# Optimization experiments

Measured on AMD Instinct MI355X. Metric: run time of the kernel, lower is better.

## Reference

```python
import jax, jax.numpy as jnp
import numpy as np

STRIDE = 2
PADDING = 1


def setup_inputs() -> dict:
    key = jax.random.key(0)
    k1, k2, k3, k4, k5 = jax.random.split(key, 5)
    B, C, H, W = 32, 128, 64, 64
    O, kh, kw = 256, 3, 3
    ah = H + 2 * PADDING - (kh - 1)  # 64
    oh = ah // STRIDE                # 32 (divisible -> ceil == floor, rest == 0)
    inputs = {
        "input": jax.random.normal(k1, (B, C, H, W), dtype=jnp.float32),
        "weight": jax.random.normal(k2, (O, C, kh, kw), dtype=jnp.float32) * 0.05,
        "bias": jax.random.normal(k3, (O,), dtype=jnp.float32) * 0.05,
        "selh": jax.random.randint(k4, (oh, oh), 0, STRIDE, dtype=jnp.int32),
        "selw": jax.random.randint(k5, (oh, oh), 0, STRIDE, dtype=jnp.int32),
    }
    return inputs


def reference(input, weight, bias, selh, selw):
    # Faithful to SConv2dAvg.forward with stoch=True, mask == -1, stride=2:
    # unfold(input, k, pad, stride=1) -> stochastic gather of one position per
    # stride x stride cell (offsets selh/selw) -> GEMM with flattened weight -> reshape.
    B, C, H, W = input.shape
    O, _, kh, kw = weight.shape
    ah = H + 2 * PADDING - (kh - 1)
    aw = W + 2 * PADDING - (kw - 1)
    oh = ah // STRIDE  # divisible by construction; ceil_mode correction is a no-op
    ow = aw // STRIDE
    xp = jnp.pad(input, ((0, 0), (0, 0), (PADDING, PADDING), (PADDING, PADDING)))
    # selected unfold positions in the afterconv grid
    rng_h = selh + (jnp.arange(oh, dtype=selh.dtype) * STRIDE)[:, None]   # [oh, ow]
    rng_w = selw + (jnp.arange(ow, dtype=selw.dtype) * STRIDE)[None, :]   # [oh, ow]
    # gather k x k patches directly (equivalent to gathering unfold columns)
    rows = rng_h[:, :, None, None] + jnp.arange(kh)[None, None, :, None]  # [oh, ow, kh, 1]
    cols = rng_w[:, :, None, None] + jnp.arange(kw)[None, None, None, :]  # [oh, ow, 1, kw]
    patches = xp[:, :, rows, cols]  # [B, C, oh, ow, kh, kw]
    out = jnp.einsum('bchwij,ocij->bohw', patches, weight) + bias[None, :, None, None]
    return out  # [B, O, oh, ow]
```

## Files before the change

kernel.cpp:

```cpp
#include <hip/hip_runtime.h>
#include <hip/hip_bf16.h>


typedef short bf16x8 __attribute__((ext_vector_type(8)));
typedef float f32x4  __attribute__((ext_vector_type(4)));

#define NSTEP 36
#define WPRE_BYTES (NSTEP * 256 * 32 * 2)
#define TRANS_BYTES (32 * 66 * 66 * 128 * 2)
#define TOTAL_WS (WPRE_BYTES + TRANS_BYTES)

__device__ __forceinline__ unsigned short f2bf(float x) {
  unsigned u = __float_as_uint(x);
  return (unsigned short)((u + 0x7fffu + ((u >> 16) & 1u)) >> 16);
}
__device__ __forceinline__ unsigned pk2(float a, float b) {
  unsigned ua = __float_as_uint(a), ub = __float_as_uint(b);
  return ((ua + 0x7fffu + ((ua >> 16) & 1u)) >> 16) |
         ((ub + 0x7fffu + ((ub >> 16) & 1u)) & 0xffff0000u);
}
__device__ __forceinline__ bf16x8 ld_frag(const uint4* a) {
  union { uint4 u; bf16x8 s; } cv; cv.u = *a; return cv.s;
}
__device__ __forceinline__ void async16(const void* g, void* l) {
  __builtin_amdgcn_global_load_lds(
      (__attribute__((address_space(1))) void*)(void*)g,
      (__attribute__((address_space(3))) void*)l, 16, 0, 0);
}

__global__ __launch_bounds__(256) void prep(const float* __restrict__ in,
                                            const float* __restrict__ w,
                                            unsigned short* __restrict__ tp,
                                            unsigned short* __restrict__ wpre) {
  const int tid = threadIdx.x;
  if (blockIdx.x >= 66) {
    const int s    = blockIdx.x - 66;
    const int o    = (blockIdx.y << 3) + (tid >> 5);
    const int k_in = tid & 31;
    const int kg   = (s << 5) + (((k_in >> 3) ^ ((o >> 1) & 3)) << 3) + (k_in & 7);
    const int tap  = kg >> 7;
    const int c    = kg & 127;
    const int di   = (tap >= 6) ? 2 : ((tap >= 3) ? 1 : 0);
    const int dj   = tap - di * 3;
    wpre[(s << 13) + (o << 5) + k_in] = f2bf(w[(o * 128 + c) * 9 + di * 3 + dj]);
    return;
  }
  __shared__ float lds[128 * 65];
  const int hp = blockIdx.x;
  const int b  = blockIdx.y;
  uint4* rowp = (uint4*)(tp + (size_t)(b * 66 + hp) * 66 * 128);
  uint4 z; z.x = z.y = z.z = z.w = 0u;
  if (hp == 0 || hp == 65) {
    for (int s = tid; s < 1056; s += 256) rowp[s] = z;
    return;
  }
  const int h = hp - 1;
  const float* src = in + ((size_t)b << 19) + (h << 6);
  const int ww4 = (tid & 15) << 2;
  const int c0  = tid >> 4;
#pragma unroll
  for (int pass = 0; pass < 8; ++pass) {
    int c = (pass << 4) + c0;
    float4 v = *(const float4*)(src + ((size_t)c << 12) + ww4);
    float* lp = lds + c * 65 + ww4;
    lp[0] = v.x; lp[1] = v.y; lp[2] = v.z; lp[3] = v.w;
  }
  __syncthreads();
  for (int s = tid; s < 1056; s += 256) {
    if (s < 16 || s >= 1040) { rowp[s] = z; continue; }
    int idx = s - 16;
    int wq = idx >> 4, c8 = idx & 15;
    const float* lp = lds + (c8 << 3) * 65 + wq;
    uint4 d;
    d.x = pk2(lp[0],   lp[65]);
    d.y = pk2(lp[130], lp[195]);
    d.z = pk2(lp[260], lp[325]);
    d.w = pk2(lp[390], lp[455]);
    rowp[s] = d;
  }
}

__global__ __launch_bounds__(512, 4) void sconv_mfma4(
    const unsigned short* __restrict__ tp,
    const unsigned short* __restrict__ wpre,
    const float* __restrict__ bias,
    const int* __restrict__ selh,
    const int* __restrict__ selw,
    float* __restrict__ out)
{
  __shared__ uint4 Alds[4][512];
  __shared__ uint4 Blds[4][512];
  __shared__ float bias_s[128];

  const int tid = threadIdx.x;
  const int d0    = blockIdx.x;
  const int blk   = ((d0 & 7) << 6) + (d0 >> 3);
  const int b     = blk >> 4;
  const int y0    = ((blk >> 1) & 7) << 2;
  const int ohalf = blk & 1;

  if (tid < 128) bias_s[tid] = bias[(ohalf << 7) + tid];

  const int p0 = tid >> 2;
  const int sl = tid & 3;
  int addr0;
  {
    const int py = y0 + (p0 >> 5);
    const int px = p0 & 31;
    addr0 = (b * 66 + 2 * py + selh[(py << 5) | px]) * 66
          + 2 * px + selw[(py << 5) | px];
  }
  const int u0 = sl ^ ((p0 >> 1) & 3);
  const char* tbase = (const char*)tp;

  const int wv = tid >> 6, ln = tid & 63;
  const int wo = wv & 1;
  const int wp = wv >> 1;
  const int lo = ln & 15, hi = ln >> 4;

  const char* wsrc = (const char*)wpre + (ohalf << 13) + (tid << 4);

  f32x4 acc[4][2] = {};

#define STAGE(BUF, KK)                                                        \
  do {                                                                        \
    const int tap_ = (KK) >> 2;                                               \
    const int di_  = (tap_ >= 6) ? 2 : ((tap_ >= 3) ? 1 : 0);                 \
    const int dj_  = tap_ - 3 * di_;                                          \
    const int toff_ = ((di_ * 66 + dj_) << 8) + (((KK) & 3) << 6) + (u0 << 4);\
    async16(tbase + ((size_t)addr0 << 8) + toff_, &Alds[BUF][wv << 6]);       \
    async16(wsrc + ((KK) << 14), &Blds[BUF][wv << 6]);                        \
  } while (0)

#define DO_MMA(BUF)                                                           \
  do {                                                                        \
    const uint4* A_ = &Alds[BUF][0];                                          \
    const uint4* B_ = &Blds[BUF][0];                                          \
    bf16x8 FW[4], FP[2];                                                      \
    _Pragma("unroll")                                                         \
    for (int f = 0; f < 4; ++f) {                                             \
      const int orow = (wo << 6) + (f << 4) + lo;                             \
      FW[f] = ld_frag(B_ + (orow << 2) + (hi ^ ((orow >> 1) & 3)));           \
    }                                                                         \
    _Pragma("unroll")                                                         \
    for (int f = 0; f < 2; ++f) {                                             \
      const int prow = (wp << 5) + (f << 4) + lo;                             \
      FP[f] = ld_frag(A_ + (prow << 2) + (hi ^ ((prow >> 1) & 3)));           \
    }                                                                         \
    _Pragma("unroll")                                                         \
    for (int fo = 0; fo < 4; ++fo)                                            \
      _Pragma("unroll")                                                       \
      for (int fp = 0; fp < 2; ++fp)                                          \
        acc[fo][fp] = __builtin_amdgcn_mfma_f32_16x16x32_bf16(                \
            FW[fo], FP[fp], acc[fo][fp], 0, 0, 0);                            \
  } while (0)

  STAGE(0, 0);
  STAGE(1, 1);

#pragma unroll 4
  for (int kk = 0; kk < NSTEP - 2; ++kk) {
    STAGE((kk + 2) & 3, kk + 2);
    asm volatile("s_waitcnt vmcnt(4)" ::: "memory");
    __builtin_amdgcn_s_barrier();
    asm volatile("" ::: "memory");
    DO_MMA(kk & 3);
    asm volatile("s_waitcnt lgkmcnt(0)" ::: "memory");
  }

  asm volatile("s_waitcnt vmcnt(2)" ::: "memory");
  __builtin_amdgcn_s_barrier();
  asm volatile("" ::: "memory");
  DO_MMA(2);
  asm volatile("s_waitcnt lgkmcnt(0)" ::: "memory");

  asm volatile("s_waitcnt vmcnt(0)" ::: "memory");
  __builtin_amdgcn_s_barrier();
  asm volatile("" ::: "memory");
  DO_MMA(3);
#undef STAGE
#undef DO_MMA

  float* ob = out + ((size_t)b << 18) + ((size_t)ohalf << 17) + (y0 << 5);
#pragma unroll
  for (int fo = 0; fo < 4; ++fo) {
    const int obase = (wo << 6) + (fo << 4) + (hi << 2);
#pragma unroll
    for (int fp = 0; fp < 2; ++fp) {
      const int pix = (wp << 5) + (fp << 4) + lo;
#pragma unroll
      for (int j = 0; j < 4; ++j) {
        const int o = obase + j;
        ob[((size_t)o << 10) + pix] = acc[fo][fp][j] + bias_s[o];
      }
    }
  }
}

__global__ __launch_bounds__(256) void sconv_naive(
    const float* __restrict__ in, const float* __restrict__ w,
    const float* __restrict__ bias, const int* __restrict__ selh,
    const int* __restrict__ selw, float* __restrict__ out) {
  int idx = (blockIdx.x << 8) + threadIdx.x;
  if (idx >= 32 * 256 * 32 * 32) return;
  int x = idx & 31, y = (idx >> 5) & 31, o = (idx >> 10) & 255, b = idx >> 18;
  int rh0 = 2 * y + selh[(y << 5) | x] - 1;
  int rw0 = 2 * x + selw[(y << 5) | x] - 1;
  const float* inb = in + ((size_t)b << 19);
  const float* wo_ = w + o * 1152;
  float acc = bias[o];
  for (int c = 0; c < 128; ++c)
    for (int i = 0; i < 3; ++i) {
      int rh = rh0 + i;
      if (rh < 0 || rh >= 64) continue;
      for (int j = 0; j < 3; ++j) {
        int rw = rw0 + j;
        if (rw < 0 || rw >= 64) continue;
        acc += inb[(c << 12) + (rh << 6) + rw] * wo_[c * 9 + i * 3 + j];
      }
    }
  out[idx] = acc;
}

extern "C" void kernel_launch(void* const* d_in, const int* in_sizes, int n_in,
                              void* d_out, int out_size, void* d_ws, size_t ws_size,
                              hipStream_t stream) {
  const float* in   = (const float*)d_in[0];
  const float* w    = (const float*)d_in[1];
  const float* bias = (const float*)d_in[2];
  const int*   selh = (const int*)d_in[3];
  const int*   selw = (const int*)d_in[4];
  float* out = (float*)d_out;

  if (ws_size >= (size_t)TOTAL_WS) {
    unsigned short* wpre = (unsigned short*)d_ws;
    unsigned short* tp   = (unsigned short*)((char*)d_ws + WPRE_BYTES);
    prep<<<dim3(102, 32), dim3(256), 0, stream>>>(in, w, tp, wpre);
    sconv_mfma4<<<dim3(512), dim3(512), 0, stream>>>(tp, wpre, bias, selh, selw, out);
  } else {
    sconv_naive<<<dim3(32768), dim3(256), 0, stream>>>(in, w, bias, selh, selw, out);
  }
}
```

Baseline: 45.31 us.

## Halve block threads and double per-wave MFMA tile with priority boost

Shrinks each block from 8 to 4 waves, with every wave now covering a 64x64 output tile (4x4 MFMA fragments) instead of 64x32. Each thread issues two A and two B async loads per stage, and the wait counts are doubled to match. The change raises operand reuse per LDS fragment load and adds s_setprio around the MFMA burst to favour math issue. In exchange it uses more accumulator registers per wave and leaves fewer waves per block to hide latency.

```diff
diff --git a/kernel.cpp b/kernel.cpp
--- a/kernel.cpp
+++ b/kernel.cpp
@@ -80,7 +80,7 @@
   }
 }
 
-__global__ __launch_bounds__(512, 4) void sconv_mfma4(
+__global__ __launch_bounds__(256, 2) void sconv_mfma5(
     const unsigned short* __restrict__ tp,
     const unsigned short* __restrict__ wpre,
     const float* __restrict__ bias,
@@ -101,58 +101,66 @@
 
   if (tid < 128) bias_s[tid] = bias[(ohalf << 7) + tid];
 
-  const int p0 = tid >> 2;
-  const int sl = tid & 3;
-  int addr0;
+  const int wv = tid >> 6, ln = tid & 63;
+
+  size_t asrc0, asrc1;
   {
-    const int py = y0 + (p0 >> 5);
-    const int px = p0 & 31;
-    addr0 = (b * 66 + 2 * py + selh[(py << 5) | px]) * 66
-          + 2 * px + selw[(py << 5) | px];
-  }
-  const int u0 = sl ^ ((p0 >> 1) & 3);
+    const int c4 = ln & 3;
+#pragma unroll
+    for (int r = 0; r < 2; ++r) {
+      const int p  = (wv << 5) + (r << 4) + (ln >> 2);
+      const int py = y0 + (p >> 5);
+      const int px = p & 31;
+      const int addr = (b * 66 + 2 * py + selh[(py << 5) | px]) * 66
+                     + 2 * px + selw[(py << 5) | px];
+      const int u = c4 ^ ((p >> 1) & 3);
+      const size_t v = ((size_t)addr << 8) + (u << 4);
+      if (r == 0) asrc0 = v; else asrc1 = v;
+    }
+  }
   const char* tbase = (const char*)tp;
-
-  const int wv = tid >> 6, ln = tid & 63;
-  const int wo = wv & 1;
-  const int wp = wv >> 1;
+  const char* wB = (const char*)wpre + (ohalf << 13) + ((wv << 1) << 10) + (ln << 4);
+
+  const int wo = wv & 1, wp = wv >> 1;
   const int lo = ln & 15, hi = ln >> 4;
 
-  const char* wsrc = (const char*)wpre + (ohalf << 13) + (tid << 4);
-
-  f32x4 acc[4][2] = {};
+  f32x4 acc[4][4] = {};
 
 #define STAGE(BUF, KK)                                                        \
   do {                                                                        \
     const int tap_ = (KK) >> 2;                                               \
     const int di_  = (tap_ >= 6) ? 2 : ((tap_ >= 3) ? 1 : 0);                 \
     const int dj_  = tap_ - 3 * di_;                                          \
-    const int toff_ = ((di_ * 66 + dj_) << 8) + (((KK) & 3) << 6) + (u0 << 4);\
-    async16(tbase + ((size_t)addr0 << 8) + toff_, &Alds[BUF][wv << 6]);       \
-    async16(wsrc + ((KK) << 14), &Blds[BUF][wv << 6]);                        \
+    const int toff_ = ((di_ * 66 + dj_) << 8) + (((KK) & 3) << 6);            \
+    async16(tbase + asrc0 + toff_, &Alds[BUF][(wv << 1) << 6]);               \
+    async16(tbase + asrc1 + toff_, &Alds[BUF][((wv << 1) + 1) << 6]);         \
+    async16(wB + ((KK) << 14),        &Blds[BUF][(wv << 1) << 6]);            \
+    async16(wB + ((KK) << 14) + 1024, &Blds[BUF][((wv << 1) + 1) << 6]);      \
   } while (0)
 
 #define DO_MMA(BUF)                                                           \
   do {                                                                        \
     const uint4* A_ = &Alds[BUF][0];                                          \
     const uint4* B_ = &Blds[BUF][0];                                          \
-    bf16x8 FW[4], FP[2];                                                      \
+    bf16x8 FW[4], FP[4];                                                      \
     _Pragma("unroll")                                                         \
     for (int f = 0; f < 4; ++f) {                                             \
       const int orow = (wo << 6) + (f << 4) + lo;                             \
       FW[f] = ld_frag(B_ + (orow << 2) + (hi ^ ((orow >> 1) & 3)));           \
     }                                                                         \
     _Pragma("unroll")                                                         \
-    for (int f = 0; f < 2; ++f) {                                             \
-      const int prow = (wp << 5) + (f << 4) + lo;                             \
+    for (int f = 0; f < 4; ++f) {                                             \
+      const int prow = (wp << 6) + (f << 4) + lo;                             \
       FP[f] = ld_frag(A_ + (prow << 2) + (hi ^ ((prow >> 1) & 3)));           \
     }                                                                         \
+    __builtin_amdgcn_s_setprio(1);                                            \
     _Pragma("unroll")                                                         \
     for (int fo = 0; fo < 4; ++fo)                                            \
       _Pragma("unroll")                                                       \
-      for (int fp = 0; fp < 2; ++fp)                                          \
+      for (int fp = 0; fp < 4; ++fp)                                          \
         acc[fo][fp] = __builtin_amdgcn_mfma_f32_16x16x32_bf16(                \
             FW[fo], FP[fp], acc[fo][fp], 0, 0, 0);                            \
+    __builtin_amdgcn_s_setprio(0);                                            \
   } while (0)
 
   STAGE(0, 0);
@@ -161,14 +169,14 @@
 #pragma unroll 4
   for (int kk = 0; kk < NSTEP - 2; ++kk) {
     STAGE((kk + 2) & 3, kk + 2);
-    asm volatile("s_waitcnt vmcnt(4)" ::: "memory");
+    asm volatile("s_waitcnt vmcnt(8)" ::: "memory");
     __builtin_amdgcn_s_barrier();
     asm volatile("" ::: "memory");
     DO_MMA(kk & 3);
     asm volatile("s_waitcnt lgkmcnt(0)" ::: "memory");
   }
 
-  asm volatile("s_waitcnt vmcnt(2)" ::: "memory");
+  asm volatile("s_waitcnt vmcnt(4)" ::: "memory");
   __builtin_amdgcn_s_barrier();
   asm volatile("" ::: "memory");
   DO_MMA(2);
@@ -186,8 +194,8 @@
   for (int fo = 0; fo < 4; ++fo) {
     const int obase = (wo << 6) + (fo << 4) + (hi << 2);
 #pragma unroll
-    for (int fp = 0; fp < 2; ++fp) {
-      const int pix = (wp << 5) + (fp << 4) + lo;
+    for (int fp = 0; fp < 4; ++fp) {
+      const int pix = (wp << 6) + (fp << 4) + lo;
 #pragma unroll
       for (int j = 0; j < 4; ++j) {
         const int o = obase + j;
@@ -236,7 +244,7 @@
     unsigned short* wpre = (unsigned short*)d_ws;
     unsigned short* tp   = (unsigned short*)((char*)d_ws + WPRE_BYTES);
     prep<<<dim3(102, 32), dim3(256), 0, stream>>>(in, w, tp, wpre);
-    sconv_mfma4<<<dim3(512), dim3(512), 0, stream>>>(tp, wpre, bias, selh, selw, out);
+    sconv_mfma5<<<dim3(512), dim3(256), 0, stream>>>(tp, wpre, bias, selh, selw, out);
   } else {
     sconv_naive<<<dim3(32768), dim3(256), 0, stream>>>(in, w, bias, selh, selw, out);
   }
```

After: 46.11 us. No clear change (+1.8%).

## Load activation fragments directly into registers, dropping the LDS A-tile

Applied to the files above, without the earlier changes.

The gathered activation operand is no longer staged through shared memory. Each lane loads its two MFMA input fragments straight from global memory into registers, double-buffered across k-steps, while weights still go through the async LDS ring. This removes the LDS writes and reads for A and cuts shared memory use. It also raises MFMA priority via s_setprio. The cost is more global loads that are less coalesced, with the 8 waves re-fetching overlapping data, and waitcnt accounting that must now cover both streams.

```diff
diff --git a/kernel.cpp b/kernel.cpp
--- a/kernel.cpp
+++ b/kernel.cpp
@@ -80,7 +80,7 @@
   }
 }
 
-__global__ __launch_bounds__(512, 4) void sconv_mfma4(
+__global__ __launch_bounds__(512, 4) void sconv_mfma6(
     const unsigned short* __restrict__ tp,
     const unsigned short* __restrict__ wpre,
     const float* __restrict__ bias,
@@ -88,7 +88,6 @@
     const int* __restrict__ selw,
     float* __restrict__ out)
 {
-  __shared__ uint4 Alds[4][512];
   __shared__ uint4 Blds[4][512];
   __shared__ float bias_s[128];
 
@@ -101,84 +100,103 @@
 
   if (tid < 128) bias_s[tid] = bias[(ohalf << 7) + tid];
 
-  const int p0 = tid >> 2;
-  const int sl = tid & 3;
-  int addr0;
-  {
-    const int py = y0 + (p0 >> 5);
-    const int px = p0 & 31;
-    addr0 = (b * 66 + 2 * py + selh[(py << 5) | px]) * 66
-          + 2 * px + selw[(py << 5) | px];
-  }
-  const int u0 = sl ^ ((p0 >> 1) & 3);
-  const char* tbase = (const char*)tp;
-
   const int wv = tid >> 6, ln = tid & 63;
   const int wo = wv & 1;
   const int wp = wv >> 1;
   const int lo = ln & 15, hi = ln >> 4;
 
-  const char* wsrc = (const char*)wpre + (ohalf << 13) + (tid << 4);
+  size_t apix0, apix1;
+  {
+#pragma unroll
+    for (int f = 0; f < 2; ++f) {
+      const int P  = (wp << 5) + (f << 4) + lo;
+      const int py = y0 + (P >> 5);
+      const int px = P & 31;
+      const int addr = (b * 66 + 2 * py + selh[(py << 5) | px]) * 66
+                     + 2 * px + selw[(py << 5) | px];
+      const size_t v = ((size_t)addr << 8) + (hi << 4);
+      if (f == 0) apix0 = v; else apix1 = v;
+    }
+  }
+  const char* tbase = (const char*)tp;
+  const char* wB = (const char*)wpre + (ohalf << 13) + (tid << 4);
 
   f32x4 acc[4][2] = {};
 
-#define STAGE(BUF, KK)                                                        \
+#define TOFF(KK) (((((KK) >> 2) >= 6 ? 2 : (((KK) >> 2) >= 3 ? 1 : 0)) * 66    \
+                   + (((KK) >> 2) - 3 * (((KK) >> 2) >= 6 ? 2                  \
+                                          : (((KK) >> 2) >= 3 ? 1 : 0)))) << 8)\
+                  + (((KK) & 3) << 6)
+
+#define LOADA(S0, S1, KK)                                                     \
   do {                                                                        \
-    const int tap_ = (KK) >> 2;                                               \
-    const int di_  = (tap_ >= 6) ? 2 : ((tap_ >= 3) ? 1 : 0);                 \
-    const int dj_  = tap_ - 3 * di_;                                          \
-    const int toff_ = ((di_ * 66 + dj_) << 8) + (((KK) & 3) << 6) + (u0 << 4);\
-    async16(tbase + ((size_t)addr0 << 8) + toff_, &Alds[BUF][wv << 6]);       \
-    async16(wsrc + ((KK) << 14), &Blds[BUF][wv << 6]);                        \
+    const int to_ = TOFF(KK);                                                 \
+    S0 = *(const bf16x8*)(tbase + apix0 + to_);                               \
+    S1 = *(const bf16x8*)(tbase + apix1 + to_);                               \
   } while (0)
 
-#define DO_MMA(BUF)                                                           \
+#define STAGE_B(KK) async16(wB + ((KK) << 14), &Blds[(KK) & 3][tid >> 2 << 2]  \
+                            + (tid & 3))
+
+#define DO_MMA(BUF, S0, S1)                                                   \
   do {                                                                        \
-    const uint4* A_ = &Alds[BUF][0];                                          \
     const uint4* B_ = &Blds[BUF][0];                                          \
-    bf16x8 FW[4], FP[2];                                                      \
+    bf16x8 FW[4];                                                             \
     _Pragma("unroll")                                                         \
     for (int f = 0; f < 4; ++f) {                                             \
       const int orow = (wo << 6) + (f << 4) + lo;                             \
       FW[f] = ld_frag(B_ + (orow << 2) + (hi ^ ((orow >> 1) & 3)));           \
     }                                                                         \
+    __builtin_amdgcn_s_setprio(1);                                            \
     _Pragma("unroll")                                                         \
-    for (int f = 0; f < 2; ++f) {                                             \
-      const int prow = (wp << 5) + (f << 4) + lo;                             \
-      FP[f] = ld_frag(A_ + (prow << 2) + (hi ^ ((prow >> 1) & 3)));           \
+    for (int fo = 0; fo < 4; ++fo) {                                          \
+      acc[fo][0] = __builtin_amdgcn_mfma_f32_16x16x32_bf16(                   \
+          FW[fo], S0, acc[fo][0], 0, 0, 0);                                   \
+      acc[fo][1] = __builtin_amdgcn_mfma_f32_16x16x32_bf16(                   \
+          FW[fo], S1, acc[fo][1], 0, 0, 0);                                   \
     }                                                                         \
-    _Pragma("unroll")                                                         \
-    for (int fo = 0; fo < 4; ++fo)                                            \
-      _Pragma("unroll")                                                       \
-      for (int fp = 0; fp < 2; ++fp)                                          \
-        acc[fo][fp] = __builtin_amdgcn_mfma_f32_16x16x32_bf16(                \
-            FW[fo], FP[fp], acc[fo][fp], 0, 0, 0);                            \
+    __builtin_amdgcn_s_setprio(0);                                            \
   } while (0)
 
-  STAGE(0, 0);
-  STAGE(1, 1);
-
-#pragma unroll 4
-  for (int kk = 0; kk < NSTEP - 2; ++kk) {
-    STAGE((kk + 2) & 3, kk + 2);
-    asm volatile("s_waitcnt vmcnt(4)" ::: "memory");
+  bf16x8 FPa0, FPa1, FPb0, FPb1;
+
+  STAGE_B(0);
+  LOADA(FPa0, FPa1, 0);
+  STAGE_B(1);
+
+#pragma unroll 2
+  for (int kk = 0; kk < NSTEP - 2; kk += 2) {
+    LOADA(FPb0, FPb1, kk + 1);
+    STAGE_B(kk + 2);
+    asm volatile("s_waitcnt vmcnt(6)" ::: "memory");
     __builtin_amdgcn_s_barrier();
     asm volatile("" ::: "memory");
-    DO_MMA(kk & 3);
+    DO_MMA(kk & 3, FPa0, FPa1);
     asm volatile("s_waitcnt lgkmcnt(0)" ::: "memory");
-  }
-
-  asm volatile("s_waitcnt vmcnt(2)" ::: "memory");
+
+    LOADA(FPa0, FPa1, kk + 2);
+    STAGE_B(kk + 3);
+    asm volatile("s_waitcnt vmcnt(6)" ::: "memory");
+    __builtin_amdgcn_s_barrier();
+    asm volatile("" ::: "memory");
+    DO_MMA((kk + 1) & 3, FPb0, FPb1);
+    asm volatile("s_waitcnt lgkmcnt(0)" ::: "memory");
+  }
+
+  LOADA(FPb0, FPb1, NSTEP - 1);
+  asm volatile("s_waitcnt vmcnt(3)" ::: "memory");
   __builtin_amdgcn_s_barrier();
   asm volatile("" ::: "memory");
-  DO_MMA(2);
+  DO_MMA(2, FPa0, FPa1);
   asm volatile("s_waitcnt lgkmcnt(0)" ::: "memory");
 
   asm volatile("s_waitcnt vmcnt(0)" ::: "memory");
   __builtin_amdgcn_s_barrier();
   asm volatile("" ::: "memory");
-  DO_MMA(3);
-#undef STAGE
+  DO_MMA(3, FPb0, FPb1);
+#undef TOFF
+#undef LOADA
+#undef STAGE_B
 #undef DO_MMA
 
   float* ob = out + ((size_t)b << 18) + ((size_t)ohalf << 17) + (y0 << 5);
@@ -236,7 +254,7 @@
     unsigned short* wpre = (unsigned short*)d_ws;
     unsigned short* tp   = (unsigned short*)((char*)d_ws + WPRE_BYTES);
     prep<<<dim3(102, 32), dim3(256), 0, stream>>>(in, w, tp, wpre);
-    sconv_mfma4<<<dim3(512), dim3(512), 0, stream>>>(tp, wpre, bias, selh, selw, out);
+    sconv_mfma6<<<dim3(512), dim3(512), 0, stream>>>(tp, wpre, bias, selh, selw, out);
   } else {
     sconv_naive<<<dim3(32768), dim3(256), 0, stream>>>(in, w, bias, selh, selw, out);
   }
```

New measurement: 63.22 us. 39.5% more time.
